# Kernel optimization log

Hardware: AMD Instinct MI355X
Metric: run time of the kernel (lower is better)

Reference implementation:

```python
import jax
jax.config.update("jax_enable_x64", True)
import jax.numpy as jnp
import numpy as np

SAMPLE_RATE = 44100
HOP = 512
B, N_MELS, T = 8, 128, 2048
L = T * HOP  # 1,048,576 samples


def _lerp_up(x, out_len):
    # torch F.interpolate(mode='linear', align_corners=True): [B,C,Tin]->[B,C,out_len]
    t_in = x.shape[-1]
    pos = jnp.arange(out_len, dtype=jnp.float64) * ((t_in - 1) / (out_len - 1))
    i0 = jnp.floor(pos).astype(jnp.int32)
    i1 = jnp.minimum(i0 + 1, t_in - 1)
    w = (pos - i0).astype(x.dtype)
    return x[..., i0] * (1 - w) + x[..., i1] * w


def _conv1d(x, w, b, pad):
    y = jax.lax.conv_general_dilated(x, w, (1,), [(pad, pad)],
                                     dimension_numbers=("NCH", "OIH", "NCH"))
    return y + b[None, :, None]


def setup_inputs() -> dict:
    key = jax.random.key(0)
    ks = jax.random.split(key, 9)
    mel_frames = jax.random.normal(ks[0], (B, N_MELS, T), dtype=jnp.float32)
    # realistic f0: 80..380 Hz
    f0_frames = 80.0 + 300.0 * jax.random.uniform(ks[1], (B, T), dtype=jnp.float32)
    noise = jax.random.normal(ks[2], (B, L), dtype=jnp.float32)
    w1 = jax.random.normal(ks[3], (128, N_MELS, 7), dtype=jnp.float32) * 0.05
    b1 = jnp.zeros((128,), jnp.float32)
    w2 = jax.random.normal(ks[4], (128, 128, 3), dtype=jnp.float32) * 0.05
    b2 = jnp.zeros((128,), jnp.float32)
    w3 = jax.random.normal(ks[5], (2, 128, 3), dtype=jnp.float32) * 0.05
    b3 = jnp.zeros((2,), jnp.float32)
    return {"mel_frames": mel_frames, "f0_frames": f0_frames, "noise": noise,
            "w1": w1, "b1": b1, "w2": w2, "b2": b2, "w3": w3, "b3": b3}


def reference(mel_frames, f0_frames, noise, w1, b1, w2, b2, w3, b3):
    # --- comb source ---
    f0 = _lerp_up(f0_frames[:, None, :], L)  # [B,1,L]
    phase = jnp.cumsum(f0.astype(jnp.float64) / SAMPLE_RATE, axis=-1)
    phase = phase - jnp.round(phase)
    phase = phase.astype(f0.dtype)
    combtooth = jnp.sinc(SAMPLE_RATE * phase / (f0 + 1e-8))[:, 0, :]  # [B,L]
    # --- magnitude network ---
    h = jax.nn.leaky_relu(_conv1d(mel_frames, w1, b1, 3), 0.2)
    h = jax.nn.leaky_relu(_conv1d(h, w2, b2, 1), 0.2)
    mags = jnp.clip(_conv1d(h, w3, b3, 1), 0.0, 1.0)  # [B,2,T]
    mags = _lerp_up(mags, L)  # [B,2,L]
    noise_sig = jnp.clip(noise * mags[:, 0, :], -1.0, 1.0)
    comb_sig = jnp.clip(combtooth * mags[:, 1, :], -1.0, 1.0)
    signal = jnp.clip(noise_sig + comb_sig, -1.0, 1.0)
    return (signal[:, None, :], (comb_sig[:, None, :], noise_sig[:, None, :]))
```

## Files before the change

### kernel.cpp

```cpp
#include <hip/hip_runtime.h>
#include <math.h>

#define BATCH 8
#define NMEL 128
#define TT 2048
#define LL 1048576
#define NCHUNK 256
#define CHUNK 4096

static constexpr double RATIO  = 2047.0 / 1048575.0;
static constexpr float  RATIOF = (float)(2047.0 / 1048575.0);
static constexpr double INV_SR = 1.0 / 44100.0;

__global__ __launch_bounds__(256) void wtrans_kernel(
    const float* __restrict__ w1, const float* __restrict__ w2,
    float* __restrict__ w1t, float* __restrict__ w2t)
{
    __shared__ float tile[32][33];
    int blk = blockIdx.x;
    const float* src; float* dst; int M, co0, m0;
    if (blk < 112) { src = w1; dst = w1t; M = 896; co0 = (blk / 28) * 32; m0 = (blk % 28) * 32; }
    else { blk -= 112; src = w2; dst = w2t; M = 384; co0 = (blk / 12) * 32; m0 = (blk % 12) * 32; }
    int tx = threadIdx.x & 31, ty = threadIdx.x >> 5;
    #pragma unroll
    for (int r = 0; r < 4; ++r)
        tile[ty + r * 8][tx] = src[(size_t)(co0 + ty + r * 8) * M + m0 + tx];
    __syncthreads();
    #pragma unroll
    for (int r = 0; r < 4; ++r)
        dst[(size_t)(m0 + ty + r * 8) * 128 + co0 + tx] = tile[tx][ty + r * 8];
}

#define XSTR 48
#define HSTR 44
__global__ __launch_bounds__(256, 3) void conv_chunk_kernel(
    const float* __restrict__ mel,
    const float* __restrict__ w1t,
    const float* __restrict__ b1,
    const float* __restrict__ w2t,
    const float* __restrict__ b2,
    const float* __restrict__ w3,
    const float* __restrict__ b3,
    float* __restrict__ mags,
    const float* __restrict__ f0f,
    double* __restrict__ sums,
    int bbase)
{
    __shared__ __align__(16) float smem[NMEL * XSTR + NMEL * HSTR];
    int tid = threadIdx.x;
    int lane = tid & 63, wid = tid >> 6;

    if (blockIdx.x >= 256) {
        int cb = blockIdx.x - 256;
        int b = bbase + (cb >> 8);
        int c = cb & (NCHUNK - 1);
        const float* row = f0f + b * TT;
        int start = c * CHUNK + tid * 16;
        double pos0 = (double)start * RATIO;
        int i0s = (int)pos0;
        float wb = (float)(pos0 - (double)i0s);
        int ib = i0s + 1 > TT - 1 ? TT - 1 : i0s + 1;
        int ic = i0s + 2 > TT - 1 ? TT - 1 : i0s + 2;
        float f0a = row[i0s], f0b = row[ib], f0c = row[ic];
        double s = 0.0;
        #pragma unroll
        for (int i = 0; i < 16; ++i) {
            float wi = wb + (float)i * RATIOF;
            bool hi = wi >= 1.0f;
            float w = hi ? wi - 1.0f : wi;
            float xa = hi ? f0b : f0a, xb = hi ? f0c : f0b;
            float f0 = xa * (1.0f - w) + xb * w;
            s += (double)f0 * INV_SR;
        }
        #pragma unroll
        for (int off = 32; off > 0; off >>= 1) s += __shfl_down(s, (unsigned)off, 64);
        double* dred = (double*)smem;
        if (lane == 0) dred[wid] = s;
        __syncthreads();
        if (tid == 0) sums[b * NCHUNK + c] = dred[0] + dred[1] + dred[2] + dred[3];
        return;
    }

    float* Xs  = smem;
    float* H1  = smem + NMEL * XSTR;
    float* H2  = smem;
    float* red = smem + NMEL * XSTR;

    int b  = bbase + (blockIdx.x >> 6);
    int t0 = (blockIdx.x & 63) * 32;
    const float* melb = mel + (size_t)b * NMEL * TT;

    #pragma unroll
    for (int it = 0; it < 6; ++it) {
        int idx = tid + it * 256;
        int ci = idx / 12, q = idx - ci * 12;
        int t = t0 - 8 + q * 4;
        float4 v = make_float4(0.f, 0.f, 0.f, 0.f);
        if (t >= 0 && t + 3 < TT) v = *(const float4*)(melb + ci * TT + t);
        *(float4*)(&Xs[ci * XSTR + q * 4]) = v;
    }
    if (tid < 128) { H1[tid * HSTR + 0] = 0.f; H1[tid * HSTR + 41] = 0.f; }
    __syncthreads();

    int cog = tid >> 3;
    int tg  = tid & 7;
    int xbase = 1 + tg * 5;

    {
        float acc[4][5];
        #pragma unroll
        for (int j = 0; j < 4; ++j) {
            float bj = b1[cog * 4 + j];
            #pragma unroll
            for (int i = 0; i < 5; ++i) acc[j][i] = bj;
        }
        #pragma unroll 2
        for (int ci = 0; ci < NMEL; ++ci) {
            float xv[11];
            #pragma unroll
            for (int i = 0; i < 11; ++i) xv[i] = Xs[ci * XSTR + xbase + i];
            const float* wr = w1t + (size_t)(ci * 7) * 128 + cog * 4;
            #pragma unroll
            for (int k = 0; k < 7; ++k) {
                float4 w4 = *(const float4*)(wr + k * 128);
                float wv[4] = {w4.x, w4.y, w4.z, w4.w};
                #pragma unroll
                for (int j = 0; j < 4; ++j)
                    #pragma unroll
                    for (int i = 0; i < 5; ++i)
                        acc[j][i] = fmaf(wv[j], xv[i + k], acc[j][i]);
            }
        }
        #pragma unroll
        for (int j = 0; j < 4; ++j)
            #pragma unroll
            for (int i = 0; i < 5; ++i) {
                int t = t0 - 4 + tg * 5 + i;
                float v = acc[j][i];
                v = v > 0.0f ? v : 0.2f * v;
                if (t < 0 || t >= TT) v = 0.0f;
                H1[(cog * 4 + j) * HSTR + 1 + tg * 5 + i] = v;
            }
    }
    __syncthreads();

    {
        float acc[4][5];
        #pragma unroll
        for (int j = 0; j < 4; ++j) {
            float bj = b2[cog * 4 + j];
            #pragma unroll
            for (int i = 0; i < 5; ++i) acc[j][i] = bj;
        }
        int hbase = tg * 5;
        #pragma unroll 2
        for (int ci = 0; ci < NMEL; ++ci) {
            float xv[7];
            #pragma unroll
            for (int i = 0; i < 7; ++i) xv[i] = H1[ci * HSTR + hbase + i];
            const float* wr = w2t + (size_t)(ci * 3) * 128 + cog * 4;
            #pragma unroll
            for (int k = 0; k < 3; ++k) {
                float4 w4 = *(const float4*)(wr + k * 128);
                float wv[4] = {w4.x, w4.y, w4.z, w4.w};
                #pragma unroll
                for (int j = 0; j < 4; ++j)
                    #pragma unroll
                    for (int i = 0; i < 5; ++i)
                        acc[j][i] = fmaf(wv[j], xv[i + k], acc[j][i]);
            }
        }
        #pragma unroll
        for (int j = 0; j < 4; ++j)
            #pragma unroll
            for (int i = 0; i < 5; ++i) {
                int t = t0 - 4 + tg * 5 + i;
                float v = acc[j][i];
                v = v > 0.0f ? v : 0.2f * v;
                if (t < 0 || t >= TT) v = 0.0f;
                H2[(cog * 4 + j) * HSTR + tg * 5 + i] = v;
            }
    }
    __syncthreads();

    {
        int o   = tid >> 7;
        int cig = (tid >> 5) & 3;
        int tt  = tid & 31;
        float a = 0.0f;
        for (int cl = 0; cl < 32; ++cl) {
            int ci = cig * 32 + cl;
            #pragma unroll
            for (int k = 0; k < 3; ++k)
                a = fmaf(w3[o * 384 + ci * 3 + k], H2[ci * HSTR + tt + 3 + k], a);
        }
        red[(o * 4 + cig) * 32 + tt] = a;
    }
    __syncthreads();
    if (tid < 64) {
        int o = tid >> 5, tt = tid & 31;
        float s = b3[o] + red[(o * 4 + 0) * 32 + tt] + red[(o * 4 + 1) * 32 + tt]
                        + red[(o * 4 + 2) * 32 + tt] + red[(o * 4 + 3) * 32 + tt];
        s = fminf(fmaxf(s, 0.0f), 1.0f);
        mags[((size_t)b * 2 + o) * TT + t0 + tt] = s;
    }
}

__device__ __forceinline__ int swz4(int g) { return g ^ ((g >> 3) & 7); }

__global__ __launch_bounds__(256, 4) void final_kernel(
    const float* __restrict__ f0f,
    const float* __restrict__ noise,
    const float* __restrict__ mags,
    const double* __restrict__ sums,
    float* __restrict__ out)
{
    int b = blockIdx.x >> 8;
    int c = blockIdx.x & (NCHUNK - 1);
    const float* row = f0f + b * TT;
    int tid = threadIdx.x;
    int lane = tid & 63, wid = tid >> 6;
    __shared__ float4 fracsV[CHUNK / 4];
    __shared__ double wsumP[4], wsumA[4];

    int chunkBase = c * CHUNK;
    int start = chunkBase + tid * 16;

    double part = (tid < c) ? sums[b * NCHUNK + tid] : 0.0;
    #pragma unroll
    for (int off = 32; off > 0; off >>= 1) part += __shfl_down(part, (unsigned)off, 64);
    if (lane == 0) wsumP[wid] = part;

    double pos0 = (double)start * RATIO;
    int i0s = (int)pos0;
    float wb = (float)(pos0 - (double)i0s);
    int ibk = i0s + 1 > TT - 1 ? TT - 1 : i0s + 1;
    int ick = i0s + 2 > TT - 1 ? TT - 1 : i0s + 2;
    float f0a = row[i0s], f0b = row[ibk], f0c = row[ick];
    float f0v[16];
    double s = 0.0;
    #pragma unroll
    for (int i = 0; i < 16; ++i) {
        float wi = wb + (float)i * RATIOF;
        bool hi = wi >= 1.0f;
        float w = hi ? wi - 1.0f : wi;
        float xa = hi ? f0b : f0a, xb = hi ? f0c : f0b;
        f0v[i] = xa * (1.0f - w) + xb * w;
        s += (double)f0v[i] * INV_SR;
    }
    double incl = s;
    #pragma unroll
    for (int off = 1; off < 64; off <<= 1) {
        double v = __shfl_up(incl, (unsigned)off, 64);
        if (lane >= off) incl += v;
    }
    if (lane == 63) wsumA[wid] = incl;
    __syncthreads();
    double run = wsumP[0] + wsumP[1] + wsumP[2] + wsumP[3] + (incl - s);
    for (int w = 0; w < wid; ++w) run += wsumA[w];

    float fb4[4];
    #pragma unroll
    for (int i = 0; i < 16; ++i) {
        run += (double)f0v[i] * INV_SR;
        double fr = run - rint(run);
        fb4[i & 3] = (float)fr;
        if ((i & 3) == 3)
            fracsV[swz4(tid * 4 + (i >> 2))] = make_float4(fb4[0], fb4[1], fb4[2], fb4[3]);
    }
    __syncthreads();

    const size_t BL = (size_t)BATCH * LL;
    const size_t outBase = (size_t)b * LL;
    const float* m0row = mags + (size_t)b * 2 * TT;
    const float* m1row = m0row + TT;

    #pragma unroll
    for (int g = 0; g < 4; ++g) {
        int G = g * 256 + tid;
        int n0 = chunkBase + G * 4;
        float4 fr4 = fracsV[swz4(G)];
        const float* frp = (const float*)&fr4;
        float4 nz4 = *(const float4*)(noise + outBase + n0);
        const float* nzp = (const float*)&nz4;

        double posg = (double)n0 * RATIO;
        int i0a = (int)posg;
        float wf = (float)(posg - (double)i0a);
        int ib = i0a + 1 > TT - 1 ? TT - 1 : i0a + 1;
        int ic = i0a + 2 > TT - 1 ? TT - 1 : i0a + 2;
        float g0a = row[i0a],   g0b = row[ib],   g0c = row[ic];
        float m0a = m0row[i0a], m0b = m0row[ib], m0c = m0row[ic];
        float m1a = m1row[i0a], m1b = m1row[ib], m1c = m1row[ic];

        float so[4], co_[4], no_[4];
        #pragma unroll
        for (int j = 0; j < 4; ++j) {
            float wj = wf + (float)j * RATIOF;
            bool hi = wj >= 1.0f;
            float w = hi ? wj - 1.0f : wj;
            float xa = hi ? g0b : g0a, xb = hi ? g0c : g0b;
            float f0 = xa * (1.0f - w) + xb * w;
            float ya = hi ? m0b : m0a, yb = hi ? m0c : m0b;
            float m0 = ya * (1.0f - w) + yb * w;
            float za = hi ? m1b : m1a, zb = hi ? m1c : m1b;
            float m1 = za * (1.0f - w) + zb * w;

            float ph = frp[j];
            float x  = 44100.0f * ph * __builtin_amdgcn_rcpf(f0 + 1e-8f);
            float px = 3.14159265358979323f * x;
            float rr = 0.5f * x;
            float rf = rr - rintf(rr);
            float sn;
            asm("v_sin_f32 %0, %1" : "=v"(sn) : "v"(rf));
            float comb = (x == 0.0f) ? 1.0f : sn * __builtin_amdgcn_rcpf(px);

            float ns = fminf(fmaxf(nzp[j] * m0, -1.0f), 1.0f);
            float cs = fminf(fmaxf(comb * m1, -1.0f), 1.0f);
            so[j] = fminf(fmaxf(ns + cs, -1.0f), 1.0f);
            co_[j] = cs; no_[j] = ns;
        }
        *(float4*)(out + outBase + n0)          = make_float4(so[0], so[1], so[2], so[3]);
        *(float4*)(out + BL + outBase + n0)     = make_float4(co_[0], co_[1], co_[2], co_[3]);
        *(float4*)(out + 2 * BL + outBase + n0) = make_float4(no_[0], no_[1], no_[2], no_[3]);
    }
}

extern "C" void kernel_launch(void* const* d_in, const int* in_sizes, int n_in,
                              void* d_out, int out_size, void* d_ws, size_t ws_size,
                              hipStream_t stream) {
    const float* mel   = (const float*)d_in[0];
    const float* f0f   = (const float*)d_in[1];
    const float* noise = (const float*)d_in[2];
    const float* w1    = (const float*)d_in[3];
    const float* b1    = (const float*)d_in[4];
    const float* w2    = (const float*)d_in[5];
    const float* b2    = (const float*)d_in[6];
    const float* w3    = (const float*)d_in[7];
    const float* b3    = (const float*)d_in[8];
    float* out = (float*)d_out;

    float* w1t  = (float*)d_ws;
    float* w2t  = w1t + 896 * 128;
    float* mags = w2t + 384 * 128;
    double* sums = (double*)(mags + BATCH * 2 * TT);

    wtrans_kernel<<<160, 256, 0, stream>>>(w1, w2, w1t, w2t);
    conv_chunk_kernel<<<256 + 4 * NCHUNK, 256, 0, stream>>>(
        mel, w1t, b1, w2t, b2, w3, b3, mags, f0f, sums, 0);
    conv_chunk_kernel<<<256 + 4 * NCHUNK, 256, 0, stream>>>(
        mel, w1t, b1, w2t, b2, w3, b3, mags, f0f, sums, 4);
    final_kernel<<<BATCH * NCHUNK, 256, 0, stream>>>(f0f, noise, mags, sums, out);
}
```

Before: 289.0 us.

## Compute phases in registers per thread and merge the two conv launches

The final kernel no longer stages phase fractions through a swizzled shared buffer behind a barrier. Each thread now handles its own 16 contiguous samples and reuses its already interpolated f0 values and mag endpoints held in registers. The two half-batch conv launches become one launch covering all batches and chunk sums, which cuts a launch and widens the grid. The trade-off is that global loads and stores in the final kernel are now strided by 64 bytes across lanes instead of fully coalesced per instruction.

```diff
diff --git a/kernel.cpp b/kernel.cpp
--- a/kernel.cpp
+++ b/kernel.cpp
@@ -43,16 +43,15 @@
     const float* __restrict__ b3,
     float* __restrict__ mags,
     const float* __restrict__ f0f,
-    double* __restrict__ sums,
-    int bbase)
+    double* __restrict__ sums)
 {
     __shared__ __align__(16) float smem[NMEL * XSTR + NMEL * HSTR];
     int tid = threadIdx.x;
     int lane = tid & 63, wid = tid >> 6;
 
-    if (blockIdx.x >= 256) {
-        int cb = blockIdx.x - 256;
-        int b = bbase + (cb >> 8);
+    if (blockIdx.x >= 512) {
+        int cb = blockIdx.x - 512;
+        int b = cb >> 8;
         int c = cb & (NCHUNK - 1);
         const float* row = f0f + b * TT;
         int start = c * CHUNK + tid * 16;
@@ -77,7 +76,7 @@
         double* dred = (double*)smem;
         if (lane == 0) dred[wid] = s;
         __syncthreads();
-        if (tid == 0) sums[b * NCHUNK + c] = dred[0] + dred[1] + dred[2] + dred[3];
+        if (tid == 0) sums[cb] = dred[0] + dred[1] + dred[2] + dred[3];
         return;
     }
 
@@ -86,7 +85,7 @@
     float* H2  = smem;
     float* red = smem + NMEL * XSTR;
 
-    int b  = bbase + (blockIdx.x >> 6);
+    int b  = blockIdx.x >> 6;
     int t0 = (blockIdx.x & 63) * 32;
     const float* melb = mel + (size_t)b * NMEL * TT;
 
@@ -205,8 +204,6 @@
         mags[((size_t)b * 2 + o) * TT + t0 + tt] = s;
     }
 }
-
-__device__ __forceinline__ int swz4(int g) { return g ^ ((g >> 3) & 7); }
 
 __global__ __launch_bounds__(256, 4) void final_kernel(
     const float* __restrict__ f0f,
@@ -220,7 +217,6 @@
     const float* row = f0f + b * TT;
     int tid = threadIdx.x;
     int lane = tid & 63, wid = tid >> 6;
-    __shared__ float4 fracsV[CHUNK / 4];
     __shared__ double wsumP[4], wsumA[4];
 
     int chunkBase = c * CHUNK;
@@ -237,6 +233,11 @@
     int ibk = i0s + 1 > TT - 1 ? TT - 1 : i0s + 1;
     int ick = i0s + 2 > TT - 1 ? TT - 1 : i0s + 2;
     float f0a = row[i0s], f0b = row[ibk], f0c = row[ick];
+    const float* m0row = mags + (size_t)b * 2 * TT;
+    const float* m1row = m0row + TT;
+    float m0a = m0row[i0s], m0b = m0row[ibk], m0c = m0row[ick];
+    float m1a = m1row[i0s], m1b = m1row[ibk], m1c = m1row[ick];
+
     float f0v[16];
     double s = 0.0;
     #pragma unroll
@@ -259,54 +260,29 @@
     double run = wsumP[0] + wsumP[1] + wsumP[2] + wsumP[3] + (incl - s);
     for (int w = 0; w < wid; ++w) run += wsumA[w];
 
-    float fb4[4];
-    #pragma unroll
-    for (int i = 0; i < 16; ++i) {
-        run += (double)f0v[i] * INV_SR;
-        double fr = run - rint(run);
-        fb4[i & 3] = (float)fr;
-        if ((i & 3) == 3)
-            fracsV[swz4(tid * 4 + (i >> 2))] = make_float4(fb4[0], fb4[1], fb4[2], fb4[3]);
-    }
-    __syncthreads();
-
     const size_t BL = (size_t)BATCH * LL;
     const size_t outBase = (size_t)b * LL;
-    const float* m0row = mags + (size_t)b * 2 * TT;
-    const float* m1row = m0row + TT;
 
     #pragma unroll
     for (int g = 0; g < 4; ++g) {
-        int G = g * 256 + tid;
-        int n0 = chunkBase + G * 4;
-        float4 fr4 = fracsV[swz4(G)];
-        const float* frp = (const float*)&fr4;
+        int n0 = start + g * 4;
         float4 nz4 = *(const float4*)(noise + outBase + n0);
         const float* nzp = (const float*)&nz4;
-
-        double posg = (double)n0 * RATIO;
-        int i0a = (int)posg;
-        float wf = (float)(posg - (double)i0a);
-        int ib = i0a + 1 > TT - 1 ? TT - 1 : i0a + 1;
-        int ic = i0a + 2 > TT - 1 ? TT - 1 : i0a + 2;
-        float g0a = row[i0a],   g0b = row[ib],   g0c = row[ic];
-        float m0a = m0row[i0a], m0b = m0row[ib], m0c = m0row[ic];
-        float m1a = m1row[i0a], m1b = m1row[ib], m1c = m1row[ic];
-
         float so[4], co_[4], no_[4];
         #pragma unroll
         for (int j = 0; j < 4; ++j) {
-            float wj = wf + (float)j * RATIOF;
-            bool hi = wj >= 1.0f;
-            float w = hi ? wj - 1.0f : wj;
-            float xa = hi ? g0b : g0a, xb = hi ? g0c : g0b;
-            float f0 = xa * (1.0f - w) + xb * w;
-            float ya = hi ? m0b : m0a, yb = hi ? m0c : m0b;
-            float m0 = ya * (1.0f - w) + yb * w;
-            float za = hi ? m1b : m1a, zb = hi ? m1c : m1b;
-            float m1 = za * (1.0f - w) + zb * w;
-
-            float ph = frp[j];
+            int i = g * 4 + j;
+            run += (double)f0v[i] * INV_SR;
+            double fr = run - rint(run);
+            float ph = (float)fr;
+
+            float wi = wb + (float)i * RATIOF;
+            bool hi = wi >= 1.0f;
+            float w = hi ? wi - 1.0f : wi;
+            float m0 = (hi ? m0b : m0a) * (1.0f - w) + (hi ? m0c : m0b) * w;
+            float m1 = (hi ? m1b : m1a) * (1.0f - w) + (hi ? m1c : m1b) * w;
+            float f0 = f0v[i];
+
             float x  = 44100.0f * ph * __builtin_amdgcn_rcpf(f0 + 1e-8f);
             float px = 3.14159265358979323f * x;
             float rr = 0.5f * x;
@@ -346,9 +322,7 @@
     double* sums = (double*)(mags + BATCH * 2 * TT);
 
     wtrans_kernel<<<160, 256, 0, stream>>>(w1, w2, w1t, w2t);
-    conv_chunk_kernel<<<256 + 4 * NCHUNK, 256, 0, stream>>>(
-        mel, w1t, b1, w2t, b2, w3, b3, mags, f0f, sums, 0);
-    conv_chunk_kernel<<<256 + 4 * NCHUNK, 256, 0, stream>>>(
-        mel, w1t, b1, w2t, b2, w3, b3, mags, f0f, sums, 4);
+    conv_chunk_kernel<<<512 + BATCH * NCHUNK, 256, 0, stream>>>(
+        mel, w1t, b1, w2t, b2, w3, b3, mags, f0f, sums);
     final_kernel<<<BATCH * NCHUNK, 256, 0, stream>>>(f0f, noise, mags, sums, out);
 }
```

After: 275.2 us. -4.8%, faster.
